# Kernel tuning notes

Hardware: AMD Instinct MI355X
Metric: run time of the kernel (lower is better)

## Reference

```python
import jax, jax.numpy as jnp
import numpy as np

I = 2048  # input_size
O = 2048  # output_size
K = 16    # number of parallel linears

def setup_inputs() -> dict:
    key = jax.random.key(0)
    ks = jax.random.split(key, 8)
    s_in = 1.0 / np.sqrt(I)
    s_cat = 1.0 / np.sqrt(K * O)
    x = jax.random.normal(ks[0], (4, 2048, I), dtype=jnp.float32)
    W16 = jax.random.uniform(ks[1], (K, O, I), jnp.float32, -s_in, s_in)   # stacked weights of 16 Linears
    b16 = jax.random.uniform(ks[2], (K, O), jnp.float32, -s_in, s_in)
    Wf = jax.random.uniform(ks[3], (O, K * O), jnp.float32, -s_cat, s_cat)  # fusion Linear weight
    bf = jax.random.uniform(ks[4], (O,), jnp.float32, -s_cat, s_cat)
    gamma = jnp.ones((O,), jnp.float32)  # LayerNorm weight
    beta = jnp.zeros((O,), jnp.float32)  # LayerNorm bias
    return {"x": x, "W16": W16, "b16": b16, "Wf": Wf, "bf": bf, "gamma": gamma, "beta": beta}

def reference(x, W16, b16, Wf, bf, gamma, beta):
    B, S, _ = x.shape
    # 16 parallel Linears as one batched GEMM; k index order == torch.cat order
    y = jnp.einsum('bsi,koi->bsko', x, W16) + b16          # [B,S,16,O]
    combined = y.reshape(B, S, K * O)                       # concat along last dim
    fused = jnp.einsum('bsc,oc->bso', combined, Wf) + bf    # fusion linear [B,S,O]
    # LayerNorm (eps=1e-5, torch default)
    mu = jnp.mean(fused, axis=-1, keepdims=True)
    var = jnp.mean(jnp.square(fused - mu), axis=-1, keepdims=True)
    normed = (fused - mu) * jax.lax.rsqrt(var + 1e-5) * gamma + beta
    # exact (erf) GELU matching torch nn.GELU default; dropout(p=0.005) is identity at eval
    return jax.nn.gelu(normed, approximate=False)
```

## Files before the change

kernel.cpp:

```cpp
#include <hip/hip_runtime.h>
#include <hip/hip_bf16.h>
#include <math.h>


typedef __bf16 bf16_t;
typedef __bf16 bf16x8 __attribute__((ext_vector_type(8)));
typedef __bf16 bf16x4 __attribute__((ext_vector_type(4)));
typedef float  f32x4  __attribute__((ext_vector_type(4)));

#define KC 32768
#define OD 2048
#define ID 2048
#define BSROWS 8192

#define GLL16(g, l) __builtin_amdgcn_global_load_lds( \
    (const __attribute__((address_space(1))) void*)(g), \
    (__attribute__((address_space(3))) void*)(l), 16, 0, 0)

__device__ __forceinline__ float wave_sum(float v) {
#pragma unroll
  for (int o = 32; o > 0; o >>= 1) v += __shfl_down(v, o, 64);
  return v;
}

__global__ __launch_bounds__(512, 1) void gemm256(
    const bf16_t* __restrict__ A, const bf16_t* __restrict__ B,
    float* __restrict__ C, int M, int N, int lda, int ldb,
    int Ks, int nbn, int mn)
{
  __shared__ char lds[131072];
  const int tid  = threadIdx.x;
  const int lane = tid & 63;
  const int wave = tid >> 6;

  const int nwg = gridDim.x;
  const int per = nwg >> 3;
  const int swz = (blockIdx.x & 7) * per + (blockIdx.x >> 3);
  const int z   = swz / mn;
  const int rem = swz - z * mn;
  const int bm  = (rem / nbn) * 256;
  const int bn  = (rem % nbn) * 256;
  const int k0  = z * Ks;
  float* Cz = C + (size_t)z * ((size_t)M * (size_t)N);

  const int wr = wave >> 2, wc = wave & 3;
  const int wrbase = wr * 128, wcbase = wc * 64;
  const int frow   = lane & 15;
  const int slot16 = (lane >> 4) * 16;

  const int srow = tid >> 2;
  const int scol = ((tid & 3) ^ ((tid >> 4) & 3)) * 8;
  const bf16_t* gA = A + (size_t)(bm + srow) * lda + k0 + scol;
  const bf16_t* gB = B + (size_t)(bn + srow) * ldb + k0 + scol;
  const int ldst = wave * 1024;

  f32x4 acc[8][4] = {};
  bf16x8 afA[8], bgA[4], afB[8], bgB[4];
  const int NC = Ks >> 5;

  const int rdswz = slot16 ^ ((lane & 12) << 2);
  const int aoff = (wrbase + frow) * 64 + rdswz;
  const int boff = (wcbase + frow) * 64 + rdswz;

#define STAGE(c) do {                                             \
    char* Ab_ = lds + (((c) & 3) << 15);                          \
    char* Bb_ = Ab_ + 16384;                                      \
    const bf16_t* a_ = gA + (size_t)(c) * 32;                     \
    const bf16_t* b_ = gB + (size_t)(c) * 32;                     \
    GLL16(a_,                     Ab_ + ldst);                    \
    GLL16(a_ + (size_t)128 * lda, Ab_ + 8192 + ldst);             \
    GLL16(b_,                     Bb_ + ldst);                    \
    GLL16(b_ + (size_t)128 * ldb, Bb_ + 8192 + ldst);             \
  } while (0)

#define READ(c, af, bg) do {                                      \
    const char* ap_ = lds + (((c) & 3) << 15) + aoff;             \
    const char* bp_ = lds + (((c) & 3) << 15) + 16384 + boff;     \
    _Pragma("unroll")                                             \
    for (int n = 0; n < 4; ++n)                                   \
      bg[n] = *reinterpret_cast<const bf16x8*>(bp_ + n * 1024);   \
    _Pragma("unroll")                                             \
    for (int m = 0; m < 8; ++m)                                   \
      af[m] = *reinterpret_cast<const bf16x8*>(ap_ + m * 1024);   \
  } while (0)

#define MFMA32(af, bg) do {                                       \
    __builtin_amdgcn_s_setprio(1);                                \
    _Pragma("unroll")                                             \
    for (int m = 0; m < 8; ++m)                                   \
      _Pragma("unroll")                                           \
      for (int n = 0; n < 4; ++n)                                 \
        acc[m][n] = __builtin_amdgcn_mfma_f32_16x16x32_bf16(      \
            af[m], bg[n], acc[m][n], 0, 0, 0);                    \
    __builtin_amdgcn_s_setprio(0);                                \
  } while (0)

#define PHASE(c, afC, bgC, afN, bgN) do {                         \
    if ((c) < NC - 3)       asm volatile("s_waitcnt vmcnt(8)" ::: "memory"); \
    else if ((c) == NC - 3) asm volatile("s_waitcnt vmcnt(4)" ::: "memory"); \
    else if ((c) == NC - 2) asm volatile("s_waitcnt vmcnt(0)" ::: "memory"); \
    __builtin_amdgcn_s_barrier();                                 \
    if ((c) + 4 < NC) STAGE((c) + 4);                             \
    if ((c) + 1 < NC) READ((c) + 1, afN, bgN);                    \
    MFMA32(afC, bgC);                                             \
  } while (0)

  STAGE(0); STAGE(1); STAGE(2); STAGE(3);
  asm volatile("s_waitcnt vmcnt(12)" ::: "memory");
  __builtin_amdgcn_s_barrier();
  READ(0, afA, bgA);

#pragma unroll 1
  for (int c = 0; c < NC; c += 2) {
    PHASE(c,     afA, bgA, afB, bgB);
    PHASE(c + 1, afB, bgB, afA, bgA);
  }
#undef PHASE
#undef MFMA32
#undef READ
#undef STAGE

  const int cr = (lane >> 4) * 4, cc = lane & 15;
#pragma unroll
  for (int m = 0; m < 8; ++m)
#pragma unroll
    for (int n = 0; n < 4; ++n) {
      size_t base = (size_t)(bm + wrbase + m * 16 + cr) * N + (bn + wcbase + n * 16 + cc);
#pragma unroll
      for (int j = 0; j < 4; ++j)
        Cz[base + (size_t)j * N] = acc[m][n][j];
    }
}

__global__ void conv_wf_beq(const float* __restrict__ Wf, const float* __restrict__ b16,
                            bf16_t* __restrict__ Wf16, float* __restrict__ beq)
{
  const int o  = blockIdx.y;
  const int cb = blockIdx.x * 2048;
  const int t  = threadIdx.x;
  const size_t gbase = (size_t)o * KC + cb + t * 8;
  const float4 v0 = *(const float4*)(Wf + gbase);
  const float4 v1 = *(const float4*)(Wf + gbase + 4);
  const float4 b0 = *(const float4*)(b16 + cb + t * 8);
  const float4 b1 = *(const float4*)(b16 + cb + t * 8 + 4);
  bf16x8 r;
  r[0] = (bf16_t)v0.x; r[1] = (bf16_t)v0.y; r[2] = (bf16_t)v0.z; r[3] = (bf16_t)v0.w;
  r[4] = (bf16_t)v1.x; r[5] = (bf16_t)v1.y; r[6] = (bf16_t)v1.z; r[7] = (bf16_t)v1.w;
  *reinterpret_cast<bf16x8*>(Wf16 + gbase) = r;
  float s = v0.x * b0.x + v0.y * b0.y + v0.z * b0.z + v0.w * b0.w
          + v1.x * b1.x + v1.y * b1.y + v1.z * b1.z + v1.w * b1.w;
  s = wave_sum(s);
  __shared__ float red[4];
  if ((t & 63) == 0) red[t >> 6] = s;
  __syncthreads();
  if (t == 0) atomicAdd(beq + o, red[0] + red[1] + red[2] + red[3]);
}

__global__ void transpose_w16(const float* __restrict__ W, bf16_t* __restrict__ T)
{
  __shared__ bf16_t tile[64][65];
  const int cb = blockIdx.x * 64;
  const int ib = blockIdx.y * 64;
  const int tx = threadIdx.x & 63;
  const int ty = threadIdx.x >> 6;
#pragma unroll
  for (int r = ty; r < 64; r += 4)
    tile[r][tx] = (bf16_t)W[(size_t)(cb + r) * ID + ib + tx];
  __syncthreads();
  const int orow = threadIdx.x >> 3;
  const int oc8  = (threadIdx.x & 7) * 8;
#pragma unroll
  for (int rr = 0; rr < 2; ++rr) {
    const int r = orow + rr * 32;
    bf16x8 v;
#pragma unroll
    for (int j = 0; j < 8; ++j) v[j] = tile[oc8 + j][r];
    *reinterpret_cast<bf16x8*>(T + (size_t)(ib + r) * KC + cb + oc8) = v;
  }
}

__global__ void conv_x(const float* __restrict__ X, bf16_t* __restrict__ X16)
{
  const size_t i = ((size_t)blockIdx.x * 256 + threadIdx.x) * 8;
  const float4 v0 = *(const float4*)(X + i);
  const float4 v1 = *(const float4*)(X + i + 4);
  bf16x8 r;
  r[0] = (bf16_t)v0.x; r[1] = (bf16_t)v0.y; r[2] = (bf16_t)v0.z; r[3] = (bf16_t)v0.w;
  r[4] = (bf16_t)v1.x; r[5] = (bf16_t)v1.y; r[6] = (bf16_t)v1.z; r[7] = (bf16_t)v1.w;
  *reinterpret_cast<bf16x8*>(X16 + i) = r;
}

__global__ void reduce_weq(const float* __restrict__ slabs, bf16_t* __restrict__ Weq)
{
  const size_t MN = (size_t)OD * ID;
  const size_t i = ((size_t)blockIdx.x * 256 + threadIdx.x) * 4;
  float4 a = *(const float4*)(slabs + i);
  float4 b = *(const float4*)(slabs + MN + i);
  float4 c = *(const float4*)(slabs + 2 * MN + i);
  float4 d = *(const float4*)(slabs + 3 * MN + i);
  bf16x4 r;
  r[0] = (bf16_t)(a.x + b.x + c.x + d.x);
  r[1] = (bf16_t)(a.y + b.y + c.y + d.y);
  r[2] = (bf16_t)(a.z + b.z + c.z + d.z);
  r[3] = (bf16_t)(a.w + b.w + c.w + d.w);
  *reinterpret_cast<bf16x4*>(Weq + i) = r;
}

__global__ __launch_bounds__(256) void ln_gelu(
    const float* __restrict__ fused, const float* __restrict__ beq,
    const float* __restrict__ bfv, const float* __restrict__ gamma,
    const float* __restrict__ beta, float* __restrict__ out)
{
  const int row = blockIdx.x;
  const int t = threadIdx.x;
  const float* fr = fused + (size_t)row * OD;
  const int c0 = t * 8;
  float v[8];
  float s = 0.f, ss = 0.f;
#pragma unroll
  for (int j = 0; j < 2; ++j) {
    float4 x  = *(const float4*)(fr  + c0 + j * 4);
    float4 bq = *(const float4*)(beq + c0 + j * 4);
    float4 bb = *(const float4*)(bfv + c0 + j * 4);
    v[j * 4 + 0] = x.x + bq.x + bb.x;
    v[j * 4 + 1] = x.y + bq.y + bb.y;
    v[j * 4 + 2] = x.z + bq.z + bb.z;
    v[j * 4 + 3] = x.w + bq.w + bb.w;
#pragma unroll
    for (int e = 0; e < 4; ++e) { float w = v[j * 4 + e]; s += w; ss += w * w; }
  }
  s = wave_sum(s); ss = wave_sum(ss);
  __shared__ float rs[4], rss[4];
  if ((t & 63) == 0) { rs[t >> 6] = s; rss[t >> 6] = ss; }
  __syncthreads();
  const float S  = rs[0] + rs[1] + rs[2] + rs[3];
  const float SS = rss[0] + rss[1] + rss[2] + rss[3];
  const float mu   = S * (1.f / OD);
  const float var  = SS * (1.f / OD) - mu * mu;
  const float rstd = rsqrtf(var + 1e-5f);
#pragma unroll
  for (int j = 0; j < 2; ++j) {
    float4 g  = *(const float4*)(gamma + c0 + j * 4);
    float4 be = *(const float4*)(beta  + c0 + j * 4);
    float4 o;
    float xn;
    xn  = (v[j * 4 + 0] - mu) * rstd * g.x + be.x; o.x = 0.5f * xn * (1.f + erff(xn * 0.70710678118f));
    xn  = (v[j * 4 + 1] - mu) * rstd * g.y + be.y; o.y = 0.5f * xn * (1.f + erff(xn * 0.70710678118f));
    xn  = (v[j * 4 + 2] - mu) * rstd * g.z + be.z; o.z = 0.5f * xn * (1.f + erff(xn * 0.70710678118f));
    xn  = (v[j * 4 + 3] - mu) * rstd * g.w + be.w; o.w = 0.5f * xn * (1.f + erff(xn * 0.70710678118f));
    *(float4*)(out + (size_t)row * OD + c0 + j * 4) = o;
  }
}

extern "C" void kernel_launch(void* const* d_in, const int* in_sizes, int n_in,
                              void* d_out, int out_size, void* d_ws, size_t ws_size,
                              hipStream_t stream) {
  const float* x     = (const float*)d_in[0];
  const float* W16   = (const float*)d_in[1];
  const float* b16   = (const float*)d_in[2];
  const float* Wf    = (const float*)d_in[3];
  const float* bfv   = (const float*)d_in[4];
  const float* gamma = (const float*)d_in[5];
  const float* beta  = (const float*)d_in[6];
  float* out = (float*)d_out;

  char* ws = (char*)d_ws;
  bf16_t* W16T  = (bf16_t*)(ws);
  bf16_t* Wf16  = (bf16_t*)(ws + 134217728);
  bf16_t* X16   = (bf16_t*)(ws + 268435456);
  bf16_t* Weq   = (bf16_t*)(ws + 301989888);
  float*  beq   = (float*)(ws + 310378496);
  float*  slabs = (float*)(ws + 310386688);
  float*  fused = slabs;

  hipMemsetAsync(beq, 0, OD * sizeof(float), stream);

  conv_wf_beq<<<dim3(16, 2048), 256, 0, stream>>>(Wf, b16, Wf16, beq);
  transpose_w16<<<dim3(KC / 64, ID / 64), 256, 0, stream>>>(W16, W16T);
  conv_x<<<(BSROWS * ID) / (256 * 8), 256, 0, stream>>>(x, X16);

  gemm256<<<256, 512, 0, stream>>>(Wf16, W16T, slabs, OD, ID, KC, KC, KC / 4, 8, 64);
  reduce_weq<<<(OD * ID) / (256 * 4), 256, 0, stream>>>(slabs, Weq);

  gemm256<<<256, 512, 0, stream>>>(X16, Weq, fused, BSROWS, OD, ID, ID, ID, 8, 256);

  ln_gelu<<<BSROWS, 256, 0, stream>>>(fused, beq, bfv, gamma, beta, out);
}
```

Baseline: 594.6 us.

## Load A fragments directly from global to registers and halve LDS for occupancy two

The GEMM now reads A-operand fragments straight from global memory into registers, two chunks ahead, and stages only B through LDS with a 4-slot, 64KB ring. Launch bounds ask for two workgroups per CU. The aim is to cut LDS traffic and footprint so two blocks can co-reside and hide latency. The costs are uncoalesced-ish direct global loads for A, more register pressure under the tighter launch bound, and a more delicate vmcnt accounting.

```diff
diff --git a/kernel.cpp b/kernel.cpp
--- a/kernel.cpp
+++ b/kernel.cpp
@@ -23,12 +23,12 @@
   return v;
 }
 
-__global__ __launch_bounds__(512, 1) void gemm256(
+__global__ __launch_bounds__(512, 2) void gemm256(
     const bf16_t* __restrict__ A, const bf16_t* __restrict__ B,
     float* __restrict__ C, int M, int N, int lda, int ldb,
     int Ks, int nbn, int mn)
 {
-  __shared__ char lds[131072];
+  __shared__ char lds[65536];
   const int tid  = threadIdx.x;
   const int lane = tid & 63;
   const int wave = tid >> 6;
@@ -45,43 +45,40 @@
 
   const int wr = wave >> 2, wc = wave & 3;
   const int wrbase = wr * 128, wcbase = wc * 64;
-  const int frow   = lane & 15;
-  const int slot16 = (lane >> 4) * 16;
+
+  const bf16_t* gAr = A + (size_t)(bm + wrbase + (lane & 15)) * lda
+                        + k0 + ((lane >> 4) * 8);
 
   const int srow = tid >> 2;
-  const int scol = ((tid & 3) ^ ((tid >> 4) & 3)) * 8;
-  const bf16_t* gA = A + (size_t)(bm + srow) * lda + k0 + scol;
-  const bf16_t* gB = B + (size_t)(bn + srow) * ldb + k0 + scol;
+  const int scol = ((tid & 3) ^ ((tid >> 2) & 3)) * 8;
+  const bf16_t* gBs = B + (size_t)(bn + srow) * ldb + k0 + scol;
   const int ldst = wave * 1024;
 
+  const int boff = (wcbase + (lane & 15)) * 64 + (((lane >> 4) ^ (lane & 3)) * 16);
+
   f32x4 acc[8][4] = {};
-  bf16x8 afA[8], bgA[4], afB[8], bgB[4];
+  bf16x8 aA[8], aB[8], bgA[4], bgB[4];
   const int NC = Ks >> 5;
 
-  const int rdswz = slot16 ^ ((lane & 12) << 2);
-  const int aoff = (wrbase + frow) * 64 + rdswz;
-  const int boff = (wcbase + frow) * 64 + rdswz;
-
-#define STAGE(c) do {                                             \
-    char* Ab_ = lds + (((c) & 3) << 15);                          \
-    char* Bb_ = Ab_ + 16384;                                      \
-    const bf16_t* a_ = gA + (size_t)(c) * 32;                     \
-    const bf16_t* b_ = gB + (size_t)(c) * 32;                     \
-    GLL16(a_,                     Ab_ + ldst);                    \
-    GLL16(a_ + (size_t)128 * lda, Ab_ + 8192 + ldst);             \
-    GLL16(b_,                     Bb_ + ldst);                    \
-    GLL16(b_ + (size_t)128 * ldb, Bb_ + 8192 + ldst);             \
-  } while (0)
-
-#define READ(c, af, bg) do {                                      \
-    const char* ap_ = lds + (((c) & 3) << 15) + aoff;             \
-    const char* bp_ = lds + (((c) & 3) << 15) + 16384 + boff;     \
+#define STAGEB(c) do {                                            \
+    char* d_ = lds + (((c) & 3) << 14);                           \
+    const bf16_t* s_ = gBs + (size_t)(c) * 32;                    \
+    GLL16(s_,                     d_ + ldst);                     \
+    GLL16(s_ + (size_t)128 * ldb, d_ + 8192 + ldst);              \
+  } while (0)
+
+#define LOADA(c, ar) do {                                         \
+    const bf16_t* p_ = gAr + (size_t)(c) * 32;                    \
+    _Pragma("unroll")                                             \
+    for (int m = 0; m < 8; ++m)                                   \
+      ar[m] = *reinterpret_cast<const bf16x8*>(p_ + (size_t)(m * 16) * lda); \
+  } while (0)
+
+#define READB(c, bg) do {                                         \
+    const char* p_ = lds + (((c) & 3) << 14) + boff;              \
     _Pragma("unroll")                                             \
     for (int n = 0; n < 4; ++n)                                   \
-      bg[n] = *reinterpret_cast<const bf16x8*>(bp_ + n * 1024);   \
-    _Pragma("unroll")                                             \
-    for (int m = 0; m < 8; ++m)                                   \
-      af[m] = *reinterpret_cast<const bf16x8*>(ap_ + m * 1024);   \
+      bg[n] = *reinterpret_cast<const bf16x8*>(p_ + n * 1024);    \
   } while (0)
 
 #define MFMA32(af, bg) do {                                       \
@@ -95,30 +92,36 @@
     __builtin_amdgcn_s_setprio(0);                                \
   } while (0)
 
-#define PHASE(c, afC, bgC, afN, bgN) do {                         \
-    if ((c) < NC - 3)       asm volatile("s_waitcnt vmcnt(8)" ::: "memory"); \
-    else if ((c) == NC - 3) asm volatile("s_waitcnt vmcnt(4)" ::: "memory"); \
-    else if ((c) == NC - 2) asm volatile("s_waitcnt vmcnt(0)" ::: "memory"); \
+#define CHUNK(c, aC, aN, bgC, bgN) do {                           \
+    if ((c) + 3 < NC) STAGEB((c) + 3);                            \
+    if ((c) + 1 < NC) READB((c) + 1, bgN);                        \
+    MFMA32(aC, bgC);                                              \
+    if ((c) + 2 < NC) LOADA((c) + 2, aC);                         \
+    if ((c) + 4 <= NC)      asm volatile("s_waitcnt vmcnt(10)" ::: "memory"); \
+    else if ((c) + 3 == NC) asm volatile("s_waitcnt vmcnt(8)"  ::: "memory"); \
+    else if ((c) + 2 == NC) asm volatile("s_waitcnt vmcnt(0)"  ::: "memory"); \
     __builtin_amdgcn_s_barrier();                                 \
-    if ((c) + 4 < NC) STAGE((c) + 4);                             \
-    if ((c) + 1 < NC) READ((c) + 1, afN, bgN);                    \
-    MFMA32(afC, bgC);                                             \
-  } while (0)
-
-  STAGE(0); STAGE(1); STAGE(2); STAGE(3);
-  asm volatile("s_waitcnt vmcnt(12)" ::: "memory");
+  } while (0)
+
+  STAGEB(0); STAGEB(1);
+  asm volatile("" ::: "memory");
+  LOADA(0, aA);
+  asm volatile("" ::: "memory");
+  STAGEB(2); LOADA(1, aB);
+  asm volatile("s_waitcnt vmcnt(10)" ::: "memory");
   __builtin_amdgcn_s_barrier();
-  READ(0, afA, bgA);
+  READB(0, bgA);
 
 #pragma unroll 1
   for (int c = 0; c < NC; c += 2) {
-    PHASE(c,     afA, bgA, afB, bgB);
-    PHASE(c + 1, afB, bgB, afA, bgA);
-  }
-#undef PHASE
+    CHUNK(c,     aA, aB, bgA, bgB);
+    CHUNK(c + 1, aB, aA, bgB, bgA);
+  }
+#undef CHUNK
 #undef MFMA32
-#undef READ
-#undef STAGE
+#undef READB
+#undef LOADA
+#undef STAGEB
 
   const int cr = (lane >> 4) * 4, cc = lane & 15;
 #pragma unroll
```

After: 992.1 us. +66.8%, slower.
